# Performance work log

Hardware: AMD Instinct MI355X
Metric: run time of the kernel (lower is better)

Reference implementation:

```python
import jax, jax.numpy as jnp
import numpy as np

B, S, D, H, R = 16, 2048, 1024, 1024, 16


def setup_inputs() -> dict:
    key = jax.random.key(0)
    ks = jax.random.split(key, 6)
    inv = 1.0 / np.sqrt(D)
    return {
        "x": jax.random.normal(ks[0], (B, S, D), jnp.float32),
        "Wa": jax.random.uniform(ks[1], (H, D), jnp.float32, -inv, inv),
        "ba": jnp.zeros((H,), jnp.float32),
        "Wg": jax.random.uniform(ks[2], (R, D), jnp.float32, -inv, inv),
        "bg": jnp.zeros((R,), jnp.float32),
        "Wu": jax.random.uniform(ks[3], (H, D), jnp.float32, -inv, inv),
        "bu": jnp.zeros((H,), jnp.float32),
        "u": jax.random.normal(ks[4], (H, R), jnp.float32) * 0.02,
        "v": jax.random.normal(ks[5], (H, R), jnp.float32) * 0.02,
    }


def reference(x, Wa, ba, Wg, bg, Wu, bu, u, v):
    # Precompute all per-step projections in big GEMMs (same math as the
    # per-step Linear calls in the original loop).
    a = jax.nn.sigmoid(jnp.einsum('bsd,hd->bsh', x, Wa) + ba)   # [B,S,H]
    g = jnp.einsum('bsd,rd->bsr', x, Wg) + bg                    # [B,S,R]
    u_in = jnp.einsum('bsd,hd->bsh', x, Wu) + bu                 # [B,S,H]

    def step(state, ins):
        a_t, g_t, u_t = ins                      # [B,H], [B,R], [B,H]
        low_rank = (state @ v) * g_t             # [B,R]
        state = a_t * state + u_t + low_rank @ u.T
        return state, None

    init = jnp.zeros((x.shape[0], Wa.shape[0]), x.dtype)
    seq = (jnp.swapaxes(a, 0, 1), jnp.swapaxes(g, 0, 1), jnp.swapaxes(u_in, 0, 1))
    state, _ = jax.lax.scan(step, init, seq)
    return state  # [B, H]
```

## Files before the change

kernel.cpp:

```cpp
#include <hip/hip_runtime.h>
#include <hip/hip_bf16.h>
#include <stdint.h>

#define Bb 16
#define Ss 2048
#define Dd 1024
#define Hh 1024
#define Rr 16
#define Mm 32768

typedef __attribute__((ext_vector_type(4))) float f32x4;
typedef __attribute__((ext_vector_type(8))) short bf16x8;

__device__ __forceinline__ unsigned short f2bf(float f) {
    union { float f; uint32_t u; } c; c.f = f;
    uint32_t u = c.u + 0x7fffu + ((c.u >> 16) & 1u);
    return (unsigned short)(u >> 16);
}
__device__ __forceinline__ float bfbits2f(uint32_t bits) {
    union { uint32_t u; float f; } c; c.u = bits << 16; return c.f;
}

__device__ __forceinline__ void gld16(const void* gsrc, void* ldst) {
    __builtin_amdgcn_global_load_lds(
        (const __attribute__((address_space(1))) unsigned int*)gsrc,
        (__attribute__((address_space(3))) unsigned int*)ldst, 16, 0, 0);
}

__device__ __forceinline__ void softbar() {
    __asm volatile("" ::: "memory");
    __builtin_amdgcn_s_waitcnt(0xC07F);
    __builtin_amdgcn_s_barrier();
    __asm volatile("" ::: "memory");
}

__global__ __launch_bounds__(256) void k_convert(
    const float* __restrict__ x, const float* __restrict__ Wa,
    const float* __restrict__ Wu,
    unsigned short* __restrict__ xb, unsigned short* __restrict__ Wab,
    unsigned short* __restrict__ Wub)
{
    long e = ((long)blockIdx.x * 256 + threadIdx.x) * 4;
    const long nx = (long)Mm * Dd;
    const long nw = (long)Hh * Dd;
    const float* src; unsigned short* dst; long o;
    if (e < nx)            { src = x;  dst = xb;  o = e; }
    else if (e < nx + nw)  { src = Wa; dst = Wab; o = e - nx; }
    else                   { src = Wu; dst = Wub; o = e - nx - nw; }
    float4 f = *(const float4*)(src + o);
    ushort4 r;
    r.x = f2bf(f.x); r.y = f2bf(f.y); r.z = f2bf(f.z); r.w = f2bf(f.w);
    *(ushort4*)(dst + o) = r;
}

__global__ __launch_bounds__(256) void k_gemm(
    const unsigned short* __restrict__ Xb,
    const unsigned short* __restrict__ Wab,
    const unsigned short* __restrict__ Wub,
    const float* __restrict__ ba, const float* __restrict__ bu,
    unsigned short* __restrict__ outA, unsigned short* __restrict__ outU)
{
    __shared__ short At[128 * 32];
    __shared__ short Bt[128 * 32];

    const int tid  = threadIdx.x;
    const int lane = tid & 63;
    const int wave = tid >> 6;
    const int bm = blockIdx.x;
    const int bn = blockIdx.y;
    const int region = bn >> 3;
    const int nbase = (bn & 7) * 128;

    const short* Ag = (const short*)Xb;
    const short* Bg = (const short*)(region ? Wub : Wab);
    const float* bias = region ? bu : ba;
    unsigned short* outp = region ? outU : outA;

    const int wm = wave & 1, wn = wave >> 1;
    const int srow = lane >> 2, sseg = lane & 3;
    const int mrow = lane & 15, kb = lane >> 4;

    f32x4 acc[4][4] = {};

    for (int kt = 0; kt < 32; ++kt) {
        __syncthreads();
        const int k0 = kt * 32;
        #pragma unroll
        for (int p = 0; p < 2; ++p) {
            const int row = p * 64 + wave * 16 + srow;
            const short* ga = Ag + (long)(bm * 128 + row) * Dd + k0 + sseg * 8;
            gld16((const void*)ga, (void*)&At[p * 2048 + wave * 512]);
            const short* gb = Bg + (long)(nbase + row) * Dd + k0 + sseg * 8;
            gld16((const void*)gb, (void*)&Bt[p * 2048 + wave * 512]);
        }
        __syncthreads();

        bf16x8 af[4], bq[4];
        #pragma unroll
        for (int i = 0; i < 4; ++i) {
            af[i] = *(const bf16x8*)&At[(wm * 64 + i * 16 + mrow) * 32 + kb * 8];
            bq[i] = *(const bf16x8*)&Bt[(wn * 64 + i * 16 + mrow) * 32 + kb * 8];
        }
        #pragma unroll
        for (int i = 0; i < 4; ++i)
            #pragma unroll
            for (int j = 0; j < 4; ++j)
                acc[i][j] = __builtin_amdgcn_mfma_f32_16x16x32_bf16(
                    af[i], bq[j], acc[i][j], 0, 0, 0);
    }

    const int col = lane & 15, rq = lane >> 4;
    #pragma unroll
    for (int j = 0; j < 4; ++j) {
        const int n = nbase + wn * 64 + j * 16 + col;
        const float bv = bias[n];
        #pragma unroll
        for (int i = 0; i < 4; ++i) {
            const int mb = bm * 128 + wm * 64 + i * 16 + rq * 4;
            #pragma unroll
            for (int r = 0; r < 4; ++r) {
                float vv = acc[i][j][r] + bv;
                if (region == 0) vv = 1.0f / (1.0f + __expf(-vv));
                outp[(long)(mb + r) * Hh + n] = f2bf(vv);
            }
        }
    }
}

__global__ __launch_bounds__(256) void k_g(
    const float* __restrict__ x, const float* __restrict__ Wg,
    const float* __restrict__ bg, float* __restrict__ g)
{
    const int tid = threadIdx.x;
    const int r = tid & 15, ml = tid >> 4;
    const long m = (long)blockIdx.x * 16 + ml;
    const float4* xr = (const float4*)(x + m * Dd);
    const float4* wr = (const float4*)(Wg + (long)r * Dd);
    float acc = 0.0f;
    #pragma unroll 4
    for (int k = 0; k < Dd / 4; ++k) {
        float4 a = xr[k], b = wr[k];
        acc = fmaf(a.x, b.x, acc); acc = fmaf(a.y, b.y, acc);
        acc = fmaf(a.z, b.z, acc); acc = fmaf(a.w, b.w, acc);
    }
    g[m * Rr + r] = acc + bg[r];
}

__global__ __launch_bounds__(1024) void k_scan(
    const unsigned short* __restrict__ a,
    const unsigned short* __restrict__ uin,
    const float* __restrict__ g,
    const float* __restrict__ u,
    const float* __restrict__ v,
    float* __restrict__ out)
{
    __shared__ __align__(16) float sbf[Hh];
    __shared__ __align__(16) float cacc[16 * 20];
    __shared__ __align__(16) float qbuf[16];

    const int tid  = threadIdx.x;
    const int lane = tid & 63;
    const int wave = tid >> 6;
    const int sub  = lane >> 4;
    const int ra   = lane & 15;
    const int b = blockIdx.x;

    const int hA = wave * 64 + sub * 16;
    float vr[16];
    #pragma unroll
    for (int j = 0; j < 16; ++j) vr[j] = v[(hA + j) * Rr + ra];
    float ur[16];
    #pragma unroll
    for (int j = 0; j < 4; ++j) {
        float4 t4 = *(const float4*)&u[tid * Rr + j * 4];
        ur[j*4+0] = t4.x; ur[j*4+1] = t4.y; ur[j*4+2] = t4.z; ur[j*4+3] = t4.w;
    }

    const unsigned short* ap = a   + (long)b * Ss * Hh + tid;
    const unsigned short* up = uin + (long)b * Ss * Hh + tid;
    const float*          gp = g   + (long)b * Ss * Rr + tid;

    float s = 0.0f;
    uint32_t pa[4], pu[4]; float pg[4];
    #pragma unroll
    for (int t = 0; t < 4; ++t) { pa[t] = ap[t * Hh]; pu[t] = up[t * Hh]; }
    ap += 4 * Hh; up += 4 * Hh;
    if (tid < 16) {
        #pragma unroll
        for (int t = 0; t < 4; ++t) pg[t] = gp[t * Rr];
        gp += 4 * Rr;
    }

    sbf[tid] = 0.0f;
    __syncthreads();

    const float* spA = &sbf[hA];

#define STEP(R, PF) do {                                                    \
                                         \
    f32x4 s0 = *(const f32x4*)(spA);                                        \
    f32x4 s1 = *((const f32x4*)(spA) + 1);                                  \
    f32x4 s2 = *((const f32x4*)(spA) + 2);                                  \
    f32x4 s3 = *((const f32x4*)(spA) + 3);                                  \
    float part = s0.x * vr[0];                                              \
    part = fmaf(s0.y, vr[1],  part); part = fmaf(s0.z, vr[2],  part);       \
    part = fmaf(s0.w, vr[3],  part); part = fmaf(s1.x, vr[4],  part);       \
    part = fmaf(s1.y, vr[5],  part); part = fmaf(s1.z, vr[6],  part);       \
    part = fmaf(s1.w, vr[7],  part); part = fmaf(s2.x, vr[8],  part);       \
    part = fmaf(s2.y, vr[9],  part); part = fmaf(s2.z, vr[10], part);       \
    part = fmaf(s2.w, vr[11], part); part = fmaf(s3.x, vr[12], part);       \
    part = fmaf(s3.y, vr[13], part); part = fmaf(s3.z, vr[14], part);       \
    part = fmaf(s3.w, vr[15], part);                                        \
    part += __shfl_xor(part, 16);                                           \
    part += __shfl_xor(part, 32);                                           \
    if (lane < 16) cacc[20 * ra + wave] = part;                             \
    softbar();                                                    \
               \
    if (tid < 16) {                                                         \
        const float* cr = &cacc[20 * tid];                                  \
        f32x4 c0 = *(const f32x4*)(cr);                                     \
        f32x4 c1 = *((const f32x4*)(cr) + 1);                               \
        f32x4 c2 = *((const f32x4*)(cr) + 2);                               \
        f32x4 c3 = *((const f32x4*)(cr) + 3);                               \
        f32x4 cs = (c0 + c1) + (c2 + c3);                                   \
        qbuf[tid] = pg[R] * ((cs.x + cs.y) + (cs.z + cs.w));                \
        if (PF) { pg[R] = *gp; gp += Rr; }                                  \
    }                                                                       \
    softbar();                                                    \
                                   \
    f32x4 q0 = *(const f32x4*)(qbuf);                                       \
    f32x4 q1 = *((const f32x4*)(qbuf) + 1);                                 \
    f32x4 q2 = *((const f32x4*)(qbuf) + 2);                                 \
    f32x4 q3 = *((const f32x4*)(qbuf) + 3);                                 \
    float lr = q0.x * ur[0];                                                \
    lr = fmaf(q0.y, ur[1],  lr); lr = fmaf(q0.z, ur[2],  lr);               \
    lr = fmaf(q0.w, ur[3],  lr); lr = fmaf(q1.x, ur[4],  lr);               \
    lr = fmaf(q1.y, ur[5],  lr); lr = fmaf(q1.z, ur[6],  lr);               \
    lr = fmaf(q1.w, ur[7],  lr); lr = fmaf(q2.x, ur[8],  lr);               \
    lr = fmaf(q2.y, ur[9],  lr); lr = fmaf(q2.z, ur[10], lr);               \
    lr = fmaf(q2.w, ur[11], lr); lr = fmaf(q3.x, ur[12], lr);               \
    lr = fmaf(q3.y, ur[13], lr); lr = fmaf(q3.z, ur[14], lr);               \
    lr = fmaf(q3.w, ur[15], lr);                                            \
    s = fmaf(bfbits2f(pa[R]), s, bfbits2f(pu[R]) + lr);                     \
    sbf[tid] = s;                                                           \
    if (PF) {                                                               \
        pa[R] = *ap; ap += Hh;                                              \
        pu[R] = *up; up += Hh;                                              \
    }                                                                       \
    softbar();                                                    \
} while (0)

    for (int t4 = 0; t4 < Ss / 4 - 1; ++t4) {
        STEP(0, 1); STEP(1, 1); STEP(2, 1); STEP(3, 1);
    }
    STEP(0, 0); STEP(1, 0); STEP(2, 0); STEP(3, 0);
#undef STEP

    out[(long)b * Hh + tid] = s;
}

extern "C" void kernel_launch(void* const* d_in, const int* in_sizes, int n_in,
                              void* d_out, int out_size, void* d_ws, size_t ws_size,
                              hipStream_t stream)
{
    const float* x  = (const float*)d_in[0];
    const float* Wa = (const float*)d_in[1];
    const float* ba = (const float*)d_in[2];
    const float* Wg = (const float*)d_in[3];
    const float* bg = (const float*)d_in[4];
    const float* Wu = (const float*)d_in[5];
    const float* bu = (const float*)d_in[6];
    const float* u  = (const float*)d_in[7];
    const float* v  = (const float*)d_in[8];
    float* out = (float*)d_out;

    char* ws = (char*)d_ws;
    unsigned short* xb   = (unsigned short*)(ws);
    unsigned short* Wab  = (unsigned short*)(ws + 67108864);
    unsigned short* Wub  = (unsigned short*)(ws + 69206016);
    unsigned short* abuf = (unsigned short*)(ws + 71303168);
    unsigned short* ubuf = (unsigned short*)(ws + 138412032);
    float*          gbuf = (float*)(ws + 205520896);

    hipLaunchKernelGGL(k_convert, dim3(34816), dim3(256), 0, stream,
                       x, Wa, Wu, xb, Wab, Wub);
    hipLaunchKernelGGL(k_gemm, dim3(256, 16), dim3(256), 0, stream,
                       xb, Wab, Wub, ba, bu, abuf, ubuf);
    hipLaunchKernelGGL(k_g, dim3(2048), dim3(256), 0, stream,
                       x, Wg, bg, gbuf);
    hipLaunchKernelGGL(k_scan, dim3(Bb), dim3(1024), 0, stream,
                       abuf, ubuf, gbuf, u, v, out);
}
```

Before: 1.912 ms.

## Cut scan step to two barriers via redundant per-wave reduction and readlane broadcast

Each wave now reduces the cross-wave partial sums itself: it reads the cacc columns, shuffle-reduces them and broadcasts the 16 low-rank coefficients with readlane. This replaces the single-thread reduction, its qbuf round trip and one of the three barriers per step. The state·v dot product is vectorised into f32x4 accumulators, the u dot product is split into four independent chains, and every thread now prefetches g. The cost is redundant reduction work and more LDS reads in every wave, in exchange for a shorter serial latency chain per timestep.

```diff
diff --git a/kernel.cpp b/kernel.cpp
--- a/kernel.cpp
+++ b/kernel.cpp
@@ -156,7 +156,6 @@
 {
     __shared__ __align__(16) float sbf[Hh];
     __shared__ __align__(16) float cacc[16 * 20];
-    __shared__ __align__(16) float qbuf[16];
 
     const int tid  = threadIdx.x;
     const int lane = tid & 63;
@@ -166,9 +165,16 @@
     const int b = blockIdx.x;
 
     const int hA = wave * 64 + sub * 16;
-    float vr[16];
-    #pragma unroll
-    for (int j = 0; j < 16; ++j) vr[j] = v[(hA + j) * Rr + ra];
+    f32x4 vr4[4];
+    #pragma unroll
+    for (int c = 0; c < 4; ++c) {
+        f32x4 t;
+        t.x = v[(hA + 4 * c + 0) * Rr + ra];
+        t.y = v[(hA + 4 * c + 1) * Rr + ra];
+        t.z = v[(hA + 4 * c + 2) * Rr + ra];
+        t.w = v[(hA + 4 * c + 3) * Rr + ra];
+        vr4[c] = t;
+    }
     float ur[16];
     #pragma unroll
     for (int j = 0; j < 4; ++j) {
@@ -178,18 +184,15 @@
 
     const unsigned short* ap = a   + (long)b * Ss * Hh + tid;
     const unsigned short* up = uin + (long)b * Ss * Hh + tid;
-    const float*          gp = g   + (long)b * Ss * Rr + tid;
+    const float*          gp = g   + (long)b * Ss * Rr + ra;
 
     float s = 0.0f;
     uint32_t pa[4], pu[4]; float pg[4];
     #pragma unroll
-    for (int t = 0; t < 4; ++t) { pa[t] = ap[t * Hh]; pu[t] = up[t * Hh]; }
-    ap += 4 * Hh; up += 4 * Hh;
-    if (tid < 16) {
-        #pragma unroll
-        for (int t = 0; t < 4; ++t) pg[t] = gp[t * Rr];
-        gp += 4 * Rr;
-    }
+    for (int t = 0; t < 4; ++t) {
+        pa[t] = ap[t * Hh]; pu[t] = up[t * Hh]; pg[t] = gp[t * Rr];
+    }
+    ap += 4 * Hh; up += 4 * Hh; gp += 4 * Rr;
 
     sbf[tid] = 0.0f;
     __syncthreads();
@@ -197,57 +200,57 @@
     const float* spA = &sbf[hA];
 
 #define STEP(R, PF) do {                                                    \
-                                         \
+            \
     f32x4 s0 = *(const f32x4*)(spA);                                        \
     f32x4 s1 = *((const f32x4*)(spA) + 1);                                  \
     f32x4 s2 = *((const f32x4*)(spA) + 2);                                  \
     f32x4 s3 = *((const f32x4*)(spA) + 3);                                  \
-    float part = s0.x * vr[0];                                              \
-    part = fmaf(s0.y, vr[1],  part); part = fmaf(s0.z, vr[2],  part);       \
-    part = fmaf(s0.w, vr[3],  part); part = fmaf(s1.x, vr[4],  part);       \
-    part = fmaf(s1.y, vr[5],  part); part = fmaf(s1.z, vr[6],  part);       \
-    part = fmaf(s1.w, vr[7],  part); part = fmaf(s2.x, vr[8],  part);       \
-    part = fmaf(s2.y, vr[9],  part); part = fmaf(s2.z, vr[10], part);       \
-    part = fmaf(s2.w, vr[11], part); part = fmaf(s3.x, vr[12], part);       \
-    part = fmaf(s3.y, vr[13], part); part = fmaf(s3.z, vr[14], part);       \
-    part = fmaf(s3.w, vr[15], part);                                        \
+    f32x4 acc = s0 * vr4[0];                                                \
+    acc = s1 * vr4[1] + acc;                                                \
+    acc = s2 * vr4[2] + acc;                                                \
+    acc = s3 * vr4[3] + acc;                                                \
+    float part = (acc.x + acc.y) + (acc.z + acc.w);                         \
     part += __shfl_xor(part, 16);                                           \
     part += __shfl_xor(part, 32);                                           \
     if (lane < 16) cacc[20 * ra + wave] = part;                             \
-    softbar();                                                    \
-               \
-    if (tid < 16) {                                                         \
-        const float* cr = &cacc[20 * tid];                                  \
-        f32x4 c0 = *(const f32x4*)(cr);                                     \
-        f32x4 c1 = *((const f32x4*)(cr) + 1);                               \
-        f32x4 c2 = *((const f32x4*)(cr) + 2);                               \
-        f32x4 c3 = *((const f32x4*)(cr) + 3);                               \
-        f32x4 cs = (c0 + c1) + (c2 + c3);                                   \
-        qbuf[tid] = pg[R] * ((cs.x + cs.y) + (cs.z + cs.w));                \
-        if (PF) { pg[R] = *gp; gp += Rr; }                                  \
-    }                                                                       \
-    softbar();                                                    \
-                                   \
-    f32x4 q0 = *(const f32x4*)(qbuf);                                       \
-    f32x4 q1 = *((const f32x4*)(qbuf) + 1);                                 \
-    f32x4 q2 = *((const f32x4*)(qbuf) + 2);                                 \
-    f32x4 q3 = *((const f32x4*)(qbuf) + 3);                                 \
-    float lr = q0.x * ur[0];                                                \
-    lr = fmaf(q0.y, ur[1],  lr); lr = fmaf(q0.z, ur[2],  lr);               \
-    lr = fmaf(q0.w, ur[3],  lr); lr = fmaf(q1.x, ur[4],  lr);               \
-    lr = fmaf(q1.y, ur[5],  lr); lr = fmaf(q1.z, ur[6],  lr);               \
-    lr = fmaf(q1.w, ur[7],  lr); lr = fmaf(q2.x, ur[8],  lr);               \
-    lr = fmaf(q2.y, ur[9],  lr); lr = fmaf(q2.z, ur[10], lr);               \
-    lr = fmaf(q2.w, ur[11], lr); lr = fmaf(q3.x, ur[12], lr);               \
-    lr = fmaf(q3.y, ur[13], lr); lr = fmaf(q3.z, ur[14], lr);               \
-    lr = fmaf(q3.w, ur[15], lr);                                            \
-    s = fmaf(bfbits2f(pa[R]), s, bfbits2f(pu[R]) + lr);                     \
-    sbf[tid] = s;                                                           \
+     \
+     \
+    float av = bfbits2f(pa[R]);                                             \
+    float uv = bfbits2f(pu[R]);                                             \
+    float gv = pg[R];                                                       \
     if (PF) {                                                               \
         pa[R] = *ap; ap += Hh;                                              \
         pu[R] = *up; up += Hh;                                              \
+        pg[R] = *gp; gp += Rr;                                              \
     }                                                                       \
-    softbar();                                                    \
+    softbar();                                      \
+        \
+    f32x4 c4 = *(const f32x4*)&cacc[20 * ra + 4 * sub];                     \
+    float qv = (c4.x + c4.y) + (c4.z + c4.w);                               \
+    qv += __shfl_xor(qv, 16);                                               \
+    qv += __shfl_xor(qv, 32);                                               \
+    qv *= gv;                                                               \
+    float qs[16];                                                           \
+    _Pragma("unroll")                                                       \
+    for (int r_ = 0; r_ < 16; ++r_)                                         \
+        qs[r_] = __int_as_float(                                            \
+            __builtin_amdgcn_readlane(__float_as_int(qv), r_));             \
+    float l0 = qs[0] * ur[0];                                               \
+    l0 = fmaf(qs[1], ur[1], l0);  l0 = fmaf(qs[2], ur[2], l0);              \
+    l0 = fmaf(qs[3], ur[3], l0);                                            \
+    float l1 = qs[4] * ur[4];                                               \
+    l1 = fmaf(qs[5], ur[5], l1);  l1 = fmaf(qs[6], ur[6], l1);              \
+    l1 = fmaf(qs[7], ur[7], l1);                                            \
+    float l2 = qs[8] * ur[8];                                               \
+    l2 = fmaf(qs[9], ur[9], l2);  l2 = fmaf(qs[10], ur[10], l2);            \
+    l2 = fmaf(qs[11], ur[11], l2);                                          \
+    float l3 = qs[12] * ur[12];                                             \
+    l3 = fmaf(qs[13], ur[13], l3); l3 = fmaf(qs[14], ur[14], l3);           \
+    l3 = fmaf(qs[15], ur[15], l3);                                          \
+    float lr = (l0 + l1) + (l2 + l3);                                       \
+    s = fmaf(av, s, uv + lr);                                               \
+    sbf[tid] = s;                                                           \
+    softbar();                                     \
 } while (0)
 
     for (int t4 = 0; t4 < Ss / 4 - 1; ++t4) {
```

New measurement: 2.139 ms. 1.12x slower.
